# Optimization experiments

Hardware: AMD Instinct MI355X
Metric: run time of the kernel (lower is better)

## Reference

```python
import jax, jax.numpy as jnp
import numpy as np

NEG_SLOPE = 0.2  # PyG GATConv default negative_slope


def _glorot(key, shape):
    fan = shape[0]
    return jax.random.normal(key, shape, dtype=jnp.float32) / np.sqrt(fan)


def setup_inputs() -> dict:
    key = jax.random.key(0)
    ks = jax.random.split(key, 32)
    N, E, C_IN, C_H, C_OUT = 20000, 320000, 128, 640, 2
    inp = {
        "x": jax.random.normal(ks[0], (N, C_IN), dtype=jnp.float32),
        "edge_index": jax.random.randint(ks[1], (2, E), 0, N, dtype=jnp.int64),
    }
    dims = [(C_IN, C_H), (C_H, C_H), (C_H, C_H), (C_H, C_H), (C_H, C_OUT)]
    for i, (ci, co) in enumerate(dims, start=1):
        k = jax.random.split(ks[1 + i], 4)
        inp[f"W{i}"] = _glorot(k[0], (ci, co))
        inp[f"as{i}"] = _glorot(k[1], (co,))
        inp[f"ad{i}"] = _glorot(k[2], (co,))
        inp[f"b{i}"] = jnp.zeros((co,), dtype=jnp.float32)
    return inp


def _gat_conv(h, W, a_src, a_dst, b, src, dst, N):
    # h: [N, Ci] -> hW: [N, Co]
    hW = h @ W
    # per-edge attention logit: LeakyReLU(alpha_src[j] + alpha_dst[i]) for edge j->i
    e = jax.nn.leaky_relu((hW @ a_src)[src] + (hW @ a_dst)[dst], NEG_SLOPE)
    # segment softmax over incoming edges of each dst node (self-loops guarantee nonempty)
    m = jax.ops.segment_max(e, dst, num_segments=N)
    ex = jnp.exp(e - m[dst])
    den = jax.ops.segment_sum(ex, dst, num_segments=N)
    alpha = ex / den[dst]
    # weighted scatter-add of source messages
    out = jax.ops.segment_sum(alpha[:, None] * hW[src], dst, num_segments=N)
    return out + b


def reference(x, edge_index, W1, as1, ad1, b1, W2, as2, ad2, b2, W3, as3, ad3, b3,
              W4, as4, ad4, b4, W5, as5, ad5, b5):
    N = x.shape[0]
    # PyG GATConv default add_self_loops=True
    loops = jnp.arange(N, dtype=edge_index.dtype)
    ei = jnp.concatenate([edge_index, jnp.stack([loops, loops])], axis=1)
    src, dst = ei[0], ei[1]
    h = jax.nn.relu(_gat_conv(x, W1, as1, ad1, b1, src, dst, N))
    h = jax.nn.relu(_gat_conv(h, W2, as2, ad2, b2, src, dst, N))
    h = jax.nn.relu(_gat_conv(h, W3, as3, ad3, b3, src, dst, N))
    h = jax.nn.relu(_gat_conv(h, W4, as4, ad4, b4, src, dst, N))
    # dropout in eval mode = identity
    return _gat_conv(h, W5, as5, ad5, b5, src, dst, N)
```

## Files before the change

kernel.cpp:

```cpp
#include <hip/hip_runtime.h>
#include <math.h>

#define N_NODES 20000
#define MPAD 20096
#define E_EDGES 320000
#define ET (E_EDGES + N_NODES)
#define C_HID 640
#define C_IN 128
#define NEG_SLOPE 0.2f

#define NXB 157
#define NYB 10
#define NXB_FULL 152
#define IDS_MAIN 1520

typedef __attribute__((ext_vector_type(8))) short bf16x8;
typedef __attribute__((ext_vector_type(4))) float f32x4;

__device__ __forceinline__ float leaky(float x) { return x > 0.f ? x : NEG_SLOPE * x; }

__device__ __forceinline__ unsigned short f2bf(float f) {
    unsigned u = __float_as_uint(f);
    unsigned r = (u + 0x7fffu + ((u >> 16) & 1u)) >> 16;
    return (unsigned short)r;
}
__device__ __forceinline__ float bf2f(unsigned short h) {
    return __uint_as_float(((unsigned)h) << 16);
}

__device__ __forceinline__ void gld16(const void* g, void* l) {
    __builtin_amdgcn_global_load_lds((const __attribute__((address_space(1))) unsigned int*)g,
                                     (__attribute__((address_space(3))) unsigned int*)l,
                                     16, 0, 0);
}

__device__ __forceinline__ void decode_xy(int id, int& bx, int& by) {
    if (id < IDS_MAIN) {
        int g = id / 80;
        bx = g * 8 + (id & 7);
        by = (id % 80) >> 3;
    } else {
        int v = id - IDS_MAIN;
        bx = NXB_FULL + v % 5;
        by = v / 5;
    }
}

__global__ void k_zero(int* p, int n) {
    int i = blockIdx.x * blockDim.x + threadIdx.x;
    if (i < n) p[i] = 0;
}

__global__ void k_count(const int* __restrict__ ei, int* __restrict__ counts) {
    int j = blockIdx.x * blockDim.x + threadIdx.x;
    if (j >= ET) return;
    int d = (j < E_EDGES) ? ei[E_EDGES + j] : (j - E_EDGES);
    atomicAdd(&counts[d], 1);
}

__global__ __launch_bounds__(1024) void k_scan(int* __restrict__ counts,
                                               int* __restrict__ rowptr) {
    __shared__ int part[1024];
    int t = threadIdx.x;
    int base = t * 20;
    int incl[20];
    int s = 0;
#pragma unroll
    for (int k = 0; k < 20; k++) {
        int i = base + k;
        int v = (i < N_NODES) ? counts[i] : 0;
        s += v;
        incl[k] = s;
    }
    part[t] = s;
    __syncthreads();
    for (int off = 1; off < 1024; off <<= 1) {
        int x = (t >= off) ? part[t - off] : 0;
        __syncthreads();
        part[t] += x;
        __syncthreads();
    }
    int prefix = (t == 0) ? 0 : part[t - 1];
    if (t == 0) rowptr[0] = 0;
#pragma unroll
    for (int k = 0; k < 20; k++) {
        int i = base + k;
        if (i < N_NODES) {
            rowptr[i + 1] = prefix + incl[k];
            counts[i] = (k == 0) ? prefix : prefix + incl[k - 1];
        }
    }
}

__global__ void k_fill(const int* __restrict__ ei, int* __restrict__ cursor, int* __restrict__ col) {
    int j = blockIdx.x * blockDim.x + threadIdx.x;
    if (j >= ET) return;
    int s, d;
    if (j < E_EDGES) { s = ei[j]; d = ei[E_EDGES + j]; }
    else { s = d = j - E_EDGES; }
    int pos = atomicAdd(&cursor[d], 1);
    col[pos] = s;
}

__global__ __launch_bounds__(256) void k_splitWT(const float* __restrict__ W,
                                                 unsigned short* __restrict__ Wth,
                                                 unsigned short* __restrict__ Wtl, int K,
                                                 float* __restrict__ zbuf, int zn) {
    if (zbuf) {
        int tid = ((blockIdx.y * gridDim.x + blockIdx.x) * 256 + threadIdx.x) * 2;
        if (tid < zn) zbuf[tid] = 0.f;
        if (tid + 1 < zn) zbuf[tid + 1] = 0.f;
    }
    __shared__ float tile[64][65];
    int t = threadIdx.x;
    int ki = blockIdx.x * 64, ni = blockIdx.y * 64;
    int tr = t >> 2;
    int tc = (t & 3) * 16;
#pragma unroll
    for (int q = 0; q < 4; ++q) {
        float4 v = *(const float4*)&W[(size_t)(ki + tr) * C_HID + ni + tc + q * 4];
        tile[tr][tc + q * 4 + 0] = v.x;
        tile[tr][tc + q * 4 + 1] = v.y;
        tile[tr][tc + q * 4 + 2] = v.z;
        tile[tr][tc + q * 4 + 3] = v.w;
    }
    __syncthreads();
    unsigned short hh[16], ll[16];
#pragma unroll
    for (int j = 0; j < 16; ++j) {
        float w = tile[tc + j][tr];
        unsigned short h = f2bf(w);
        hh[j] = h;
        ll[j] = f2bf(w - bf2f(h));
    }
    size_t o = (size_t)(ni + tr) * K + ki + tc;
#pragma unroll
    for (int q = 0; q < 4; ++q) {
        *(ushort4*)&Wth[o + q * 4] = make_ushort4(hh[q*4], hh[q*4+1], hh[q*4+2], hh[q*4+3]);
        *(ushort4*)&Wtl[o + q * 4] = make_ushort4(ll[q*4], ll[q*4+1], ll[q*4+2], ll[q*4+3]);
    }
}

__global__ void k_padzero(unsigned short* __restrict__ xah, unsigned short* __restrict__ xal,
                          unsigned short* __restrict__ ph, unsigned short* __restrict__ pl) {
    int idx = blockIdx.x * blockDim.x + threadIdx.x;
    const int nx = (MPAD - N_NODES) * C_IN;
    const int np = (MPAD - N_NODES) * C_HID;
    if (idx < nx) {
        xah[N_NODES * C_IN + idx] = 0;
        xal[N_NODES * C_IN + idx] = 0;
    }
    if (idx < np) {
        ph[N_NODES * C_HID + idx] = 0;
        pl[N_NODES * C_HID + idx] = 0;
    }
}

__global__ void k_wa(const float* __restrict__ W, const float* __restrict__ a_s,
                     const float* __restrict__ a_d,
                     float* __restrict__ ws_, float* __restrict__ wd_) {
    int wave = (blockIdx.x * blockDim.x + threadIdx.x) >> 6;
    int lane = threadIdx.x & 63;
    if (wave >= C_IN) return;
    const float* row = W + (size_t)wave * C_HID;
    float s = 0.f, d = 0.f;
#pragma unroll
    for (int c = lane; c < C_HID; c += 64) {
        float w = row[c];
        s = fmaf(w, a_s[c], s);
        d = fmaf(w, a_d[c], d);
    }
    for (int o = 32; o; o >>= 1) { s += __shfl_xor(s, o); d += __shfl_xor(d, o); }
    if (lane == 0) { ws_[wave] = s; wd_[wave] = d; }
}

__global__ __launch_bounds__(256) void k_logitx(const float* __restrict__ x,
                                                const float* __restrict__ ws_,
                                                const float* __restrict__ wd_,
                                                float* __restrict__ as_, float* __restrict__ ad_) {
    int wave = (blockIdx.x * blockDim.x + threadIdx.x) >> 6;
    int lane = threadIdx.x & 63;
    if (wave >= N_NODES) return;
    float2 xv = ((const float2*)(x + (size_t)wave * C_IN))[lane];
    float2 wsv = ((const float2*)ws_)[lane];
    float2 wdv = ((const float2*)wd_)[lane];
    float s = xv.x * wsv.x + xv.y * wsv.y;
    float d = xv.x * wdv.x + xv.y * wdv.y;
    for (int o = 32; o; o >>= 1) { s += __shfl_xor(s, o); d += __shfl_xor(d, o); }
    if (lane == 0) { as_[wave] = s; ad_[wave] = d; }
}

__global__ __launch_bounds__(256) void k_alpha(const float* __restrict__ as_,
                                               const float* __restrict__ ad_,
                                               const int* __restrict__ rowptr,
                                               const int* __restrict__ col,
                                               float* __restrict__ alpha) {
    int wave = (blockIdx.x * blockDim.x + threadIdx.x) >> 6;
    int lane = threadIdx.x & 63;
    if (wave >= N_NODES) return;
    int start = rowptr[wave], end = rowptr[wave + 1];
    float adi = ad_[wave];
    float m = -1e30f;
    for (int j = start + lane; j < end; j += 64)
        m = fmaxf(m, leaky(as_[col[j]] + adi));
    for (int o = 32; o; o >>= 1) m = fmaxf(m, __shfl_xor(m, o));
    float den = 0.f;
    for (int j = start + lane; j < end; j += 64)
        den += __expf(leaky(as_[col[j]] + adi) - m);
    for (int o = 32; o; o >>= 1) den += __shfl_xor(den, o);
    float inv = 1.f / den;
    for (int j = start + lane; j < end; j += 64)
        alpha[j] = __expf(leaky(as_[col[j]] + adi) - m) * inv;
}

__global__ __launch_bounds__(256) void k_mfma_gemm(
    const unsigned short* __restrict__ Ahi, const unsigned short* __restrict__ Alo,
    const unsigned short* __restrict__ Bth, const unsigned short* __restrict__ Btl,
    float* __restrict__ C, int K, int M,
    const float* __restrict__ asrc, const float* __restrict__ adst,
    float* __restrict__ as_, float* __restrict__ ad_) {
    __shared__ unsigned short lds[24576];
    const int t = threadIdx.x;
    const int lane = t & 63, wv = t >> 6;
    const int wm = wv >> 1, wn = wv & 1;
    const int quad = lane >> 4, cl = lane & 15;
    int bx, by;
    decode_xy(blockIdx.x, bx, by);
    const int rowBase = bx * 128;
    const int colBase = by * 64;
    const int sr = t >> 3;
    const int scg = ((t & 7) ^ (sr & 7)) * 8;

    f32x4 acc[4][2];
#pragma unroll
    for (int i = 0; i < 4; i++)
#pragma unroll
        for (int j = 0; j < 2; j++)
            acc[i][j] = (f32x4){0.f, 0.f, 0.f, 0.f};

    for (int k0 = 0; k0 < K; k0 += 64) {
        __syncthreads();
#pragma unroll
        for (int p = 0; p < 4; ++p) {
            int r = p * 32 + sr;
            size_t ga = (size_t)(rowBase + r) * K + k0 + scg;
            int lo = p * 2048 + t * 8;
            gld16(Ahi + ga, &lds[lo]);
            gld16(Alo + ga, &lds[8192 + lo]);
        }
#pragma unroll
        for (int p = 0; p < 2; ++p) {
            int r = p * 32 + sr;
            size_t gb = (size_t)(colBase + r) * K + k0 + scg;
            int lo = p * 2048 + t * 8;
            gld16(Bth + gb, &lds[16384 + lo]);
            gld16(Btl + gb, &lds[20480 + lo]);
        }
        __syncthreads();

#pragma unroll
        for (int ks = 0; ks < 2; ++ks) {
            bf16x8 ah[4], al[4], bh[2], bl[2];
#pragma unroll
            for (int i = 0; i < 4; ++i) {
                int row = wm * 64 + i * 16 + cl;
                int am = row * 64 + (((ks * 4 + quad) ^ (row & 7)) * 8);
                ah[i] = *(const bf16x8*)&lds[am];
                al[i] = *(const bf16x8*)&lds[8192 + am];
            }
#pragma unroll
            for (int j = 0; j < 2; ++j) {
                int row = wn * 32 + j * 16 + cl;
                int bn = row * 64 + (((ks * 4 + quad) ^ (row & 7)) * 8);
                bh[j] = *(const bf16x8*)&lds[16384 + bn];
                bl[j] = *(const bf16x8*)&lds[20480 + bn];
            }
#pragma unroll
            for (int i = 0; i < 4; ++i)
#pragma unroll
                for (int j = 0; j < 2; ++j) {
                    acc[i][j] = __builtin_amdgcn_mfma_f32_16x16x32_bf16(ah[i], bh[j], acc[i][j], 0, 0, 0);
                    acc[i][j] = __builtin_amdgcn_mfma_f32_16x16x32_bf16(ah[i], bl[j], acc[i][j], 0, 0, 0);
                    acc[i][j] = __builtin_amdgcn_mfma_f32_16x16x32_bf16(al[i], bh[j], acc[i][j], 0, 0, 0);
                }
        }
    }

#pragma unroll
    for (int i = 0; i < 4; ++i)
#pragma unroll
        for (int j = 0; j < 2; ++j) {
            int colC = colBase + wn * 32 + j * 16 + cl;
#pragma unroll
            for (int rr = 0; rr < 4; ++rr) {
                int rowC = rowBase + wm * 64 + i * 16 + quad * 4 + rr;
                if (rowC < M) C[(size_t)rowC * C_HID + colC] = acc[i][j][rr];
            }
        }

    float av[2], dv[2];
#pragma unroll
    for (int j = 0; j < 2; ++j) {
        int cn = colBase + wn * 32 + j * 16 + cl;
        av[j] = asrc[cn];
        dv[j] = adst[cn];
    }
#pragma unroll
    for (int i = 0; i < 4; ++i)
#pragma unroll
        for (int rr = 0; rr < 4; ++rr) {
            float s = 0.f, d = 0.f;
#pragma unroll
            for (int j = 0; j < 2; ++j) {
                float v = acc[i][j][rr];
                s = fmaf(v, av[j], s);
                d = fmaf(v, dv[j], d);
            }
#pragma unroll
            for (int o = 8; o >= 1; o >>= 1) {
                s += __shfl_xor(s, o);
                d += __shfl_xor(d, o);
            }
            int rowC = rowBase + wm * 64 + i * 16 + quad * 4 + rr;
            if (cl == 0 && rowC < M) {
                atomicAdd(&as_[rowC], s);
                atomicAdd(&ad_[rowC], d);
            }
        }
}

__global__ __launch_bounds__(256) void k_mfma_gemm_pair(
    const unsigned short* __restrict__ Ahi, const unsigned short* __restrict__ Alo,
    const unsigned short* __restrict__ Bth, const unsigned short* __restrict__ Btl,
    unsigned short* __restrict__ Oh, unsigned short* __restrict__ Ol,
    const float* __restrict__ bias, int K, int M) {
    __shared__ unsigned short lds[24576];
    const int t = threadIdx.x;
    const int lane = t & 63, wv = t >> 6;
    const int wm = wv >> 1, wn = wv & 1;
    const int quad = lane >> 4, cl = lane & 15;
    int bx, by;
    decode_xy(blockIdx.x, bx, by);
    const int rowBase = bx * 128;
    const int colBase = by * 64;
    const int sr = t >> 3;
    const int scg = ((t & 7) ^ (sr & 7)) * 8;

    f32x4 acc[4][2];
#pragma unroll
    for (int i = 0; i < 4; i++)
#pragma unroll
        for (int j = 0; j < 2; j++)
            acc[i][j] = (f32x4){0.f, 0.f, 0.f, 0.f};

    for (int k0 = 0; k0 < K; k0 += 64) {
        __syncthreads();
#pragma unroll
        for (int p = 0; p < 4; ++p) {
            int r = p * 32 + sr;
            size_t ga = (size_t)(rowBase + r) * K + k0 + scg;
            int lo = p * 2048 + t * 8;
            gld16(Ahi + ga, &lds[lo]);
            gld16(Alo + ga, &lds[8192 + lo]);
        }
#pragma unroll
        for (int p = 0; p < 2; ++p) {
            int r = p * 32 + sr;
            size_t gb = (size_t)(colBase + r) * K + k0 + scg;
            int lo = p * 2048 + t * 8;
            gld16(Bth + gb, &lds[16384 + lo]);
            gld16(Btl + gb, &lds[20480 + lo]);
        }
        __syncthreads();

#pragma unroll
        for (int ks = 0; ks < 2; ++ks) {
            bf16x8 ah[4], al[4], bh[2], bl[2];
#pragma unroll
            for (int i = 0; i < 4; ++i) {
                int row = wm * 64 + i * 16 + cl;
                int am = row * 64 + (((ks * 4 + quad) ^ (row & 7)) * 8);
                ah[i] = *(const bf16x8*)&lds[am];
                al[i] = *(const bf16x8*)&lds[8192 + am];
            }
#pragma unroll
            for (int j = 0; j < 2; ++j) {
                int row = wn * 32 + j * 16 + cl;
                int bn = row * 64 + (((ks * 4 + quad) ^ (row & 7)) * 8);
                bh[j] = *(const bf16x8*)&lds[16384 + bn];
                bl[j] = *(const bf16x8*)&lds[20480 + bn];
            }
#pragma unroll
            for (int i = 0; i < 4; ++i)
#pragma unroll
                for (int j = 0; j < 2; ++j) {
                    acc[i][j] = __builtin_amdgcn_mfma_f32_16x16x32_bf16(ah[i], bh[j], acc[i][j], 0, 0, 0);
                    acc[i][j] = __builtin_amdgcn_mfma_f32_16x16x32_bf16(ah[i], bl[j], acc[i][j], 0, 0, 0);
                    acc[i][j] = __builtin_amdgcn_mfma_f32_16x16x32_bf16(al[i], bh[j], acc[i][j], 0, 0, 0);
                }
        }
    }

#pragma unroll
    for (int j = 0; j < 2; ++j) {
        int colC = colBase + wn * 32 + j * 16 + cl;
        float bv = bias[colC];
#pragma unroll
        for (int i = 0; i < 4; ++i)
#pragma unroll
            for (int rr = 0; rr < 4; ++rr) {
                int rowC = rowBase + wm * 64 + i * 16 + quad * 4 + rr;
                if (rowC < M) {
                    float v = fmaxf(acc[i][j][rr] + bv, 0.f);
                    unsigned short h = f2bf(v);
                    Oh[(size_t)rowC * C_HID + colC] = h;
                    Ol[(size_t)rowC * C_HID + colC] = f2bf(v - bf2f(h));
                }
            }
    }
}

__global__ __launch_bounds__(256) void k_gather64(const float* __restrict__ hW,
                                                  const float* __restrict__ alpha,
                                                  const int* __restrict__ rowptr,
                                                  const int* __restrict__ col,
                                                  const float* __restrict__ bias,
                                                  unsigned short* __restrict__ outh,
                                                  unsigned short* __restrict__ outl) {
    int lane = threadIdx.x & 63;
    int node = __builtin_amdgcn_readfirstlane(blockIdx.x * 4 + (threadIdx.x >> 6));
    int c = blockIdx.y;
    if (node >= N_NODES) return;
    int start = rowptr[node], end = rowptr[node + 1];
    const float* base = hW + c * 64 + lane;
    float ax = 0.f;

    int j0 = start;
    for (; j0 + 16 <= end; j0 += 16) {
        int cv[16];
        float av[16];
#pragma unroll
        for (int q = 0; q < 16; ++q) { cv[q] = col[j0 + q]; av[q] = alpha[j0 + q]; }
        float r[16];
#pragma unroll
        for (int q = 0; q < 16; ++q) r[q] = base[(size_t)cv[q] * C_HID];
#pragma unroll
        for (int q = 0; q < 16; ++q) ax = fmaf(av[q], r[q], ax);
    }
    if (j0 < end) {
        int jb = end - 16; if (jb < 0) jb = 0;
        int cv[16];
        float av[16];
#pragma unroll
        for (int q = 0; q < 16; ++q) {
            cv[q] = col[jb + q];
            av[q] = (jb + q >= j0) ? alpha[jb + q] : 0.f;
        }
        float r[16];
#pragma unroll
        for (int q = 0; q < 16; ++q) r[q] = base[(size_t)cv[q] * C_HID];
#pragma unroll
        for (int q = 0; q < 16; ++q) ax = fmaf(av[q], r[q], ax);
    }

    float v0 = fmaxf(ax + bias[c * 64 + lane], 0.f);
    unsigned short h0 = f2bf(v0);
    size_t o = (size_t)node * C_HID + c * 64 + lane;
    outh[o] = h0;
    outl[o] = f2bf(v0 - bf2f(h0));
}

__global__ __launch_bounds__(256) void k_gather_x(const float* __restrict__ x,
                                                  const float* __restrict__ as_,
                                                  const float* __restrict__ ad_,
                                                  const int* __restrict__ rowptr,
                                                  const int* __restrict__ col,
                                                  unsigned short* __restrict__ outh,
                                                  unsigned short* __restrict__ outl) {
    int wv = threadIdx.x >> 6, lane = threadIdx.x & 63;
    int node = blockIdx.x * 4 + wv;
    if (node >= N_NODES) return;
    int start = rowptr[node], end = rowptr[node + 1];
    int deg = end - start;
    const float* base = x + lane * 2;
    float ax = 0.f, ay = 0.f;
    float adi = ad_[node];

    if (deg <= 64) {
        int col_v = col[start + min(lane, deg - 1)];
        float asv = as_[col_v];
        float logit = (lane < deg) ? leaky(asv + adi) : -1e30f;
        float m = logit;
#pragma unroll
        for (int o = 32; o; o >>= 1) m = fmaxf(m, __shfl_xor(m, o));
        float ex = __expf(logit - m);
        float den = ex;
#pragma unroll
        for (int o = 32; o; o >>= 1) den += __shfl_xor(den, o);
        float alpha_v = ex / den;

        for (int e0 = 0; e0 < deg; e0 += 8) {
            float2 r[8];
            float a[8];
#pragma unroll
            for (int q = 0; q < 8; ++q) {
                int e = e0 + q;
                int ec = min(e, deg - 1);
                int s = __shfl(col_v, ec);
                float ar = __shfl(alpha_v, ec);
                a[q] = (e < deg) ? ar : 0.f;
                r[q] = *(const float2*)(base + (size_t)s * C_IN);
            }
#pragma unroll
            for (int q = 0; q < 8; ++q) {
                ax = fmaf(a[q], r[q].x, ax);
                ay = fmaf(a[q], r[q].y, ay);
            }
        }
    } else {
        float m = -1e30f;
        for (int j = start + lane; j < end; j += 64)
            m = fmaxf(m, leaky(as_[col[j]] + adi));
        for (int o = 32; o; o >>= 1) m = fmaxf(m, __shfl_xor(m, o));
        float den = 0.f;
        for (int j = start + lane; j < end; j += 64)
            den += __expf(leaky(as_[col[j]] + adi) - m);
        for (int o = 32; o; o >>= 1) den += __shfl_xor(den, o);
        float inv = 1.f / den;
        for (int j = start; j < end; ++j) {
            int s = col[j];
            float a = __expf(leaky(as_[s] + adi) - m) * inv;
            float2 r = *(const float2*)(base + (size_t)s * C_IN);
            ax = fmaf(a, r.x, ax);
            ay = fmaf(a, r.y, ay);
        }
    }

    unsigned short h0 = f2bf(ax), h1 = f2bf(ay);
    size_t o = (size_t)node * C_IN + lane * 2;
    *(ushort2*)&outh[o] = make_ushort2(h0, h1);
    *(ushort2*)&outl[o] = make_ushort2(f2bf(ax - bf2f(h0)), f2bf(ay - bf2f(h1)));
}

__global__ __launch_bounds__(256) void k_gemm2(const unsigned short* __restrict__ hh,
                                               const unsigned short* __restrict__ hl,
                                               const float* __restrict__ W,
                                               const float* __restrict__ asrc,
                                               const float* __restrict__ adst,
                                               float* __restrict__ hW5,
                                               float* __restrict__ as_,
                                               float* __restrict__ ad_) {
    int wave = (blockIdx.x * blockDim.x + threadIdx.x) >> 6;
    int lane = threadIdx.x & 63;
    if (wave >= N_NODES) return;
    const ushort2* rh = (const ushort2*)(hh + (size_t)wave * C_HID);
    const ushort2* rl = (const ushort2*)(hl + (size_t)wave * C_HID);
    float a0 = 0.f, a1 = 0.f;
#pragma unroll
    for (int k2 = lane; k2 < C_HID / 2; k2 += 64) {
        ushort2 h2 = rh[k2];
        ushort2 l2 = rl[k2];
        float v0 = bf2f(h2.x) + bf2f(l2.x);
        float v1 = bf2f(h2.y) + bf2f(l2.y);
        int k = k2 * 2;
        a0 = fmaf(v0, W[k * 2 + 0], a0);
        a1 = fmaf(v0, W[k * 2 + 1], a1);
        a0 = fmaf(v1, W[k * 2 + 2], a0);
        a1 = fmaf(v1, W[k * 2 + 3], a1);
    }
    for (int o = 32; o; o >>= 1) { a0 += __shfl_xor(a0, o); a1 += __shfl_xor(a1, o); }
    if (lane == 0) {
        hW5[wave * 2 + 0] = a0;
        hW5[wave * 2 + 1] = a1;
        as_[wave] = a0 * asrc[0] + a1 * asrc[1];
        ad_[wave] = a0 * adst[0] + a1 * adst[1];
    }
}

__global__ __launch_bounds__(256) void k_agg2(const float* __restrict__ hW5,
                                              const float* __restrict__ as_,
                                              const float* __restrict__ ad_,
                                              const int* __restrict__ rowptr,
                                              const int* __restrict__ col,
                                              const float* __restrict__ bias,
                                              float* __restrict__ out) {
    int wv = threadIdx.x >> 6, lane = threadIdx.x & 63;
    int node = blockIdx.x * 4 + wv;
    if (node >= N_NODES) return;
    int start = rowptr[node], end = rowptr[node + 1];
    int deg = end - start;
    float adi = ad_[node];
    float o0, o1;
    if (deg <= 64) {
        int cv = col[start + min(lane, deg - 1)];
        float logit = (lane < deg) ? leaky(as_[cv] + adi) : -1e30f;
        float m = logit;
#pragma unroll
        for (int o = 32; o; o >>= 1) m = fmaxf(m, __shfl_xor(m, o));
        float ex = __expf(logit - m);
        float den = ex;
#pragma unroll
        for (int o = 32; o; o >>= 1) den += __shfl_xor(den, o);
        float al = ex / den;
        float2 hv = make_float2(0.f, 0.f);
        if (lane < deg) hv = *(const float2*)&hW5[cv * 2];
        o0 = al * hv.x; o1 = al * hv.y;
#pragma unroll
        for (int o = 32; o; o >>= 1) { o0 += __shfl_xor(o0, o); o1 += __shfl_xor(o1, o); }
    } else {
        float m = -1e30f;
        for (int j = start + lane; j < end; j += 64)
            m = fmaxf(m, leaky(as_[col[j]] + adi));
        for (int o = 32; o; o >>= 1) m = fmaxf(m, __shfl_xor(m, o));
        float den = 0.f;
        for (int j = start + lane; j < end; j += 64)
            den += __expf(leaky(as_[col[j]] + adi) - m);
        for (int o = 32; o; o >>= 1) den += __shfl_xor(den, o);
        float inv = 1.f / den;
        o0 = 0.f; o1 = 0.f;
        for (int j = start + lane; j < end; j += 64) {
            int s = col[j];
            float al = __expf(leaky(as_[s] + adi) - m) * inv;
            o0 = fmaf(al, hW5[s * 2 + 0], o0);
            o1 = fmaf(al, hW5[s * 2 + 1], o1);
        }
        for (int o = 32; o; o >>= 1) { o0 += __shfl_xor(o0, o); o1 += __shfl_xor(o1, o); }
    }
    if (lane == 0) {
        out[node * 2 + 0] = o0 + bias[0];
        out[node * 2 + 1] = o1 + bias[1];
    }
}

extern "C" void kernel_launch(void* const* d_in, const int* in_sizes, int n_in,
                              void* d_out, int out_size, void* d_ws, size_t ws_size,
                              hipStream_t stream) {
    const float* x   = (const float*)d_in[0];
    const int*   ei  = (const int*)d_in[1];
    const float* W[5]  = {(const float*)d_in[2],  (const float*)d_in[6],
                          (const float*)d_in[10], (const float*)d_in[14],
                          (const float*)d_in[18]};
    const float* As[5] = {(const float*)d_in[3],  (const float*)d_in[7],
                          (const float*)d_in[11], (const float*)d_in[15],
                          (const float*)d_in[19]};
    const float* Ad[5] = {(const float*)d_in[4],  (const float*)d_in[8],
                          (const float*)d_in[12], (const float*)d_in[16],
                          (const float*)d_in[20]};
    const float* Bi[5] = {(const float*)d_in[5],  (const float*)d_in[9],
                          (const float*)d_in[13], (const float*)d_in[17],
                          (const float*)d_in[21]};
    float* out = (float*)d_out;

    char* w = (char*)d_ws;
    float* bufX = (float*)w;                 w += (size_t)N_NODES * C_HID * 4;
    unsigned short* xa_hi = (unsigned short*)bufX;
    unsigned short* xa_lo = xa_hi + (size_t)MPAD * C_IN;
    unsigned short* pair_hi = (unsigned short*)w; w += (size_t)MPAD * C_HID * 2;
    unsigned short* pair_lo = (unsigned short*)w; w += (size_t)MPAD * C_HID * 2;
    unsigned short* Wth = (unsigned short*)w;     w += (size_t)C_HID * C_HID * 2;
    unsigned short* Wtl = (unsigned short*)w;     w += (size_t)C_HID * C_HID * 2;
    float* as_  = (float*)w;  w += N_NODES * 4;
    float* ad_  = (float*)w;  w += N_NODES * 4;
    float* hW5  = (float*)w;  w += N_NODES * 2 * 4;
    float* ws_  = (float*)w;  w += C_IN * 4;
    float* wd_  = (float*)w;  w += C_IN * 4;
    float* alpha = (float*)w; w += ET * 4;
    int* rowptr = (int*)w;    w += (N_NODES + 1) * 4 + 12;
    int* counts = (int*)w;    w += N_NODES * 4;
    int* col    = (int*)w;    w += ET * 4;

    const int TB = 256;
    k_zero<<<(N_NODES + TB - 1) / TB, TB, 0, stream>>>(counts, N_NODES);
    k_count<<<(ET + TB - 1) / TB, TB, 0, stream>>>(ei, counts);
    k_scan<<<1, 1024, 0, stream>>>(counts, rowptr);
    k_fill<<<(ET + TB - 1) / TB, TB, 0, stream>>>(ei, counts, col);

    k_padzero<<<((MPAD - N_NODES) * C_HID + TB - 1) / TB, TB, 0, stream>>>(xa_hi, xa_lo, pair_hi, pair_lo);

    const int gemmBlocks = NXB * NYB;
    dim3 gathGrid(N_NODES / 4, 10);
    int nodeWaveBlocks = (N_NODES + 3) / 4;

    k_splitWT<<<dim3(C_IN / 64, C_HID / 64), TB, 0, stream>>>(W[0], Wth, Wtl, C_IN, (float*)0, 0);
    k_wa<<<32, TB, 0, stream>>>(W[0], As[0], Ad[0], ws_, wd_);
    k_logitx<<<nodeWaveBlocks, TB, 0, stream>>>(x, ws_, wd_, as_, ad_);
    k_gather_x<<<nodeWaveBlocks, TB, 0, stream>>>(x, as_, ad_, rowptr, col, xa_hi, xa_lo);
    k_mfma_gemm_pair<<<gemmBlocks, TB, 0, stream>>>(xa_hi, xa_lo, Wth, Wtl,
                                                    pair_hi, pair_lo, Bi[0], C_IN, N_NODES);

    for (int l = 1; l <= 3; ++l) {
        k_splitWT<<<dim3(C_HID / 64, C_HID / 64), TB, 0, stream>>>(W[l], Wth, Wtl, C_HID,
                                                                   as_, 2 * N_NODES);
        k_mfma_gemm<<<gemmBlocks, TB, 0, stream>>>(pair_hi, pair_lo, Wth, Wtl, bufX, C_HID, N_NODES,
                                                   As[l], Ad[l], as_, ad_);
        k_alpha<<<nodeWaveBlocks, TB, 0, stream>>>(as_, ad_, rowptr, col, alpha);
        k_gather64<<<gathGrid, TB, 0, stream>>>(bufX, alpha, rowptr, col, Bi[l], pair_hi, pair_lo);
    }

    k_gemm2<<<nodeWaveBlocks, TB, 0, stream>>>(pair_hi, pair_lo, W[4], As[4], Ad[4], hW5, as_, ad_);
    k_agg2<<<nodeWaveBlocks, TB, 0, stream>>>(hW5, as_, ad_, rowptr, col, Bi[4], out);
}
```

Before: 715.1 us.

## Gather two nodes per wave with 32-channel halves in layer aggregation

Result: slower. 1.010 ms (+41.3%).

```diff
diff --git a/kernel.cpp b/kernel.cpp
--- a/kernel.cpp
+++ b/kernel.cpp
@@ -94,7 +94,10 @@
 
 __global__ void k_fill(const int* __restrict__ ei, int* __restrict__ cursor, int* __restrict__ col) {
     int j = blockIdx.x * blockDim.x + threadIdx.x;
-    if (j >= ET) return;
+    if (j >= ET) {
+        if (j < ET + 16) col[j] = 0;
+        return;
+    }
     int s, d;
     if (j < E_EDGES) { s = ei[j]; d = ei[E_EDGES + j]; }
     else { s = d = j - E_EDGES; }
@@ -420,7 +423,7 @@
     }
 }
 
-__global__ __launch_bounds__(256) void k_gather64(const float* __restrict__ hW,
+__global__ __launch_bounds__(256) void k_gather32(const float* __restrict__ hW,
                                                   const float* __restrict__ alpha,
                                                   const int* __restrict__ rowptr,
                                                   const int* __restrict__ col,
@@ -428,44 +431,43 @@
                                                   unsigned short* __restrict__ outh,
                                                   unsigned short* __restrict__ outl) {
     int lane = threadIdx.x & 63;
-    int node = __builtin_amdgcn_readfirstlane(blockIdx.x * 4 + (threadIdx.x >> 6));
+    int half = lane >> 5;
+    int cl = lane & 31;
+    int pairId = __builtin_amdgcn_readfirstlane(blockIdx.x * 4 + (threadIdx.x >> 6));
     int c = blockIdx.y;
-    if (node >= N_NODES) return;
-    int start = rowptr[node], end = rowptr[node + 1];
-    const float* base = hW + c * 64 + lane;
+    int nodeA = pairId * 2;
+    int sA = rowptr[nodeA], eA = rowptr[nodeA + 1], eB = rowptr[nodeA + 2];
+    int degA = eA - sA, degB = eB - eA;
+    int G = (max(degA, degB) + 15) >> 4;
+    const float* base = hW + c * 32 + cl;
     float ax = 0.f;
 
-    int j0 = start;
-    for (; j0 + 16 <= end; j0 += 16) {
-        int cv[16];
-        float av[16];
-#pragma unroll
-        for (int q = 0; q < 16; ++q) { cv[q] = col[j0 + q]; av[q] = alpha[j0 + q]; }
-        float r[16];
-#pragma unroll
-        for (int q = 0; q < 16; ++q) r[q] = base[(size_t)cv[q] * C_HID];
-#pragma unroll
-        for (int q = 0; q < 16; ++q) ax = fmaf(av[q], r[q], ax);
-    }
-    if (j0 < end) {
-        int jb = end - 16; if (jb < 0) jb = 0;
-        int cv[16];
-        float av[16];
+    for (int g = 0; g < G; ++g) {
+        int jA = sA + g * 16, jB = eA + g * 16;
+        int cvA[16], cvB[16];
+        float avA[16], avB[16];
 #pragma unroll
         for (int q = 0; q < 16; ++q) {
-            cv[q] = col[jb + q];
-            av[q] = (jb + q >= j0) ? alpha[jb + q] : 0.f;
-        }
-        float r[16];
-#pragma unroll
-        for (int q = 0; q < 16; ++q) r[q] = base[(size_t)cv[q] * C_HID];
-#pragma unroll
-        for (int q = 0; q < 16; ++q) ax = fmaf(av[q], r[q], ax);
-    }
-
-    float v0 = fmaxf(ax + bias[c * 64 + lane], 0.f);
+            cvA[q] = col[jA + q];
+            cvB[q] = col[jB + q];
+            avA[q] = (jA + q < eA) ? alpha[jA + q] : 0.f;
+            avB[q] = (jB + q < eB) ? alpha[jB + q] : 0.f;
+        }
+        float r[16], a[16];
+#pragma unroll
+        for (int q = 0; q < 16; ++q) {
+            int s = half ? cvB[q] : cvA[q];
+            a[q] = half ? avB[q] : avA[q];
+            r[q] = base[(size_t)s * C_HID];
+        }
+#pragma unroll
+        for (int q = 0; q < 16; ++q) ax = fmaf(a[q], r[q], ax);
+    }
+
+    int node = nodeA + half;
+    float v0 = fmaxf(ax + bias[c * 32 + cl], 0.f);
     unsigned short h0 = f2bf(v0);
-    size_t o = (size_t)node * C_HID + c * 64 + lane;
+    size_t o = (size_t)node * C_HID + c * 32 + cl;
     outh[o] = h0;
     outl[o] = f2bf(v0 - bf2f(h0));
 }
@@ -664,21 +666,21 @@
     float* hW5  = (float*)w;  w += N_NODES * 2 * 4;
     float* ws_  = (float*)w;  w += C_IN * 4;
     float* wd_  = (float*)w;  w += C_IN * 4;
-    float* alpha = (float*)w; w += ET * 4;
+    float* alpha = (float*)w; w += (ET + 16) * 4;
     int* rowptr = (int*)w;    w += (N_NODES + 1) * 4 + 12;
     int* counts = (int*)w;    w += N_NODES * 4;
-    int* col    = (int*)w;    w += ET * 4;
+    int* col    = (int*)w;    w += (ET + 16) * 4;
 
     const int TB = 256;
     k_zero<<<(N_NODES + TB - 1) / TB, TB, 0, stream>>>(counts, N_NODES);
     k_count<<<(ET + TB - 1) / TB, TB, 0, stream>>>(ei, counts);
     k_scan<<<1, 1024, 0, stream>>>(counts, rowptr);
-    k_fill<<<(ET + TB - 1) / TB, TB, 0, stream>>>(ei, counts, col);
+    k_fill<<<(ET + 16 + TB - 1) / TB, TB, 0, stream>>>(ei, counts, col);
 
     k_padzero<<<((MPAD - N_NODES) * C_HID + TB - 1) / TB, TB, 0, stream>>>(xa_hi, xa_lo, pair_hi, pair_lo);
 
     const int gemmBlocks = NXB * NYB;
-    dim3 gathGrid(N_NODES / 4, 10);
+    dim3 gathGrid(N_NODES / 8, 20);
     int nodeWaveBlocks = (N_NODES + 3) / 4;
 
     k_splitWT<<<dim3(C_IN / 64, C_HID / 64), TB, 0, stream>>>(W[0], Wth, Wtl, C_IN, (float*)0, 0);
@@ -694,7 +696,7 @@
         k_mfma_gemm<<<gemmBlocks, TB, 0, stream>>>(pair_hi, pair_lo, Wth, Wtl, bufX, C_HID, N_NODES,
                                                    As[l], Ad[l], as_, ad_);
         k_alpha<<<nodeWaveBlocks, TB, 0, stream>>>(as_, ad_, rowptr, col, alpha);
-        k_gather64<<<gathGrid, TB, 0, stream>>>(bufX, alpha, rowptr, col, Bi[l], pair_hi, pair_lo);
+        k_gather32<<<gathGrid, TB, 0, stream>>>(bufX, alpha, rowptr, col, Bi[l], pair_hi, pair_lo);
     }
 
     k_gemm2<<<nodeWaveBlocks, TB, 0, stream>>>(pair_hi, pair_lo, W[4], As[4], Ad[4], hW5, as_, ad_);
```
